# Performance work log

Hardware: AMD Instinct MI355X
Metric: run time of the kernel (lower is better)

The kernel has to match this reference:

```python
import jax, jax.numpy as jnp
import numpy as np

B, C, K, P = 32, 32, 3, 4
PSIZE = P * P
STRIDE = 2
EPS = 1e-8
BN_EPS = 1e-5


def _bn(x, scale, bias, mean, var):
    # eval-mode BatchNorm over channel-last axis
    return (x - mean) * (scale / jnp.sqrt(var + BN_EPS)) + bias


def setup_inputs() -> dict:
    key = jax.random.key(0)
    ks = jax.random.split(key, 13)
    b, h, w = 8, 64, 64
    c1_in, c1_out = C * K * K * 16, C * K * K      # 4608 -> 288
    c2_in, c2_out = C * K * K * 17, C * 17         # 4896 -> 544
    return {
        "x": jax.random.normal(ks[0], (b, B * (PSIZE + 1), h, w), jnp.float32),
        "weights": jax.random.normal(ks[1], (1, 1, C, B + 1), jnp.float32),
        "gamma": jax.random.normal(ks[2], (1, 1, 1, B, 1), jnp.float32),
        "conv1_w": jax.random.normal(ks[3], (c1_out, c1_in), jnp.float32) * 0.02,
        "bn1_scale": jax.random.uniform(ks[4], (c1_out,), jnp.float32) + 0.5,
        "bn1_bias": jax.random.normal(ks[5], (c1_out,), jnp.float32) * 0.1,
        "bn1_mean": jax.random.normal(ks[6], (c1_out,), jnp.float32) * 0.1,
        "bn1_var": jax.random.uniform(ks[7], (c1_out,), jnp.float32) + 0.5,
        "conv2_w": jax.random.normal(ks[8], (c2_out, c2_in), jnp.float32) * 0.02,
        "bn2_scale": jax.random.uniform(ks[9], (c2_out,), jnp.float32) + 0.5,
        "bn2_bias": jax.random.normal(ks[10], (c2_out,), jnp.float32) * 0.1,
        "bn2_mean": jax.random.normal(ks[11], (c2_out,), jnp.float32) * 0.1,
        "bn2_var": jax.random.uniform(ks[12], (c2_out,), jnp.float32) + 0.5,
    }


def reference(x, weights, gamma, conv1_w, bn1_scale, bn1_bias, bn1_mean, bn1_var,
              conv2_w, bn2_scale, bn2_bias, bn2_mean, bn2_var):
    b = x.shape[0]
    x = jnp.transpose(x, (0, 2, 3, 1))                       # (b,h,w,c)
    # add_pathes: zero-pad h,w by 1 then gather K*K overlapping patches
    x = jnp.pad(x, ((0, 0), (1, 1), (1, 1), (0, 0)))
    hp = x.shape[1]
    starts = np.arange(0, hp - K + 1, STRIDE)                # static
    idxs = starts[:, None] + np.arange(K)                    # (oh,K)
    oh = ow = int((hp - K) / STRIDE + 1)
    x = x[:, idxs]                                           # (b,oh,K,wp,c)
    x = x[:, :, :, idxs]                                     # (b,oh,K,ow,K,c)
    x = jnp.transpose(x, (0, 1, 3, 2, 4, 5))                 # (b,oh,ow,K,K,c)

    hw, kk = oh * ow, K * K
    p_in = x[..., :B * PSIZE].reshape(b, hw, kk, B, PSIZE)
    p_in = jnp.transpose(p_in, (0, 3, 1, 2, 4)).reshape(b, B, hw * kk * PSIZE)
    a_in = x[..., B * PSIZE:].reshape(b, hw, kk, B, 1)

    # transform_view: per-capsule-type normalization over all patches
    mu = p_in.mean(-1, keepdims=True)
    var = p_in.var(-1, ddof=1, keepdims=True)                # torch unbiased var
    p = (p_in - mu) / jnp.sqrt(var + EPS)                    # (b,B,N)
    p = jnp.transpose(p, (0, 2, 1)).reshape(b, hw, kk, B, PSIZE)
    p = a_in * p * gamma                                     # activation+gamma gating
    gsm = jax.nn.softmax(gamma, axis=3)                      # softmax over B
    psum = jnp.sum(p * gsm, axis=3, keepdims=True)           # (b,hw,kk,1,PSIZE)
    p = jnp.concatenate([p, psum], axis=3)                   # (b,hw,kk,B+1,PSIZE)
    w_sm = jax.nn.softmax(weights, axis=2)[0, 0]             # (C,B+1), softmax over C
    p_out = jnp.einsum('cd,bhkdp->bhkcp', w_sm, p)           # (b,hw,kk,C,PSIZE)
    p_out = p_out.reshape(b, oh, ow, kk * C * PSIZE)         # channels-last, 4608

    # conv1: 1x1 conv + BN + sigmoid
    a = jnp.einsum('bhwc,oc->bhwo', p_out, conv1_w)
    a = jax.nn.sigmoid(_bn(a, bn1_scale, bn1_bias, bn1_mean, bn1_var))
    out = jnp.concatenate([p_out, a], axis=3)                # 4896 channels
    # conv2: 1x1 conv + BN + relu
    y = jnp.einsum('bhwc,oc->bhwo', out, conv2_w)
    y = jax.nn.relu(_bn(y, bn2_scale, bn2_bias, bn2_mean, bn2_var))
    return jnp.transpose(y, (0, 3, 1, 2))                    # (b, C*17, oh, ow)
```

## Files before the change

### kernel.cpp

```cpp
#include <hip/hip_runtime.h>
#include <math.h>


typedef unsigned short u16;
typedef __attribute__((ext_vector_type(8))) short short8;
typedef __attribute__((ext_vector_type(4))) float f32x4;
typedef __attribute__((ext_vector_type(16))) float f32x16;

#define MFMA16(a, b, c) __builtin_amdgcn_mfma_f32_16x16x32_bf16(a, b, c, 0, 0, 0)
#define MFMA32(a, b, c) __builtin_amdgcn_mfma_f32_32x32x16_bf16(a, b, c, 0, 0, 0)
#define SB0() __builtin_amdgcn_sched_barrier(0)

#define LN_EPS 1e-8f

#define O_MU    0
#define O_RSTD  256
#define O_W2    512
#define O_BN1S  1536
#define O_BN1B  1824
#define O_BN2S  2112
#define O_BN2B  2656
#define O_ZB    3200

#define O_G_B     16384ull
#define O_AACT_B  (O_G_B + 33554432ull)
#define O_PART_B  (O_AACT_B + 5242880ull)
#define O_WF_B    (O_PART_B + 17825792ull)
#define O_WA_B    (O_WF_B + 9437184ull)

__device__ __forceinline__ u16 f2bf(float f) {
  union { float f; unsigned u; } v; v.f = f;
  unsigned r = (v.u + 0x7fffu + ((v.u >> 16) & 1u)) >> 16;
  return (u16)r;
}

__device__ __forceinline__ void gll16(const void* g, void* l) {
  __builtin_amdgcn_global_load_lds(
      (const __attribute__((address_space(1))) unsigned int*)g,
      (__attribute__((address_space(3))) unsigned int*)l, 16, 0, 0);
}

__device__ __forceinline__ int sfun(int r) { return (r >> 1) & 3; }

__global__ __launch_bounds__(256) void prep_kernel(
    const float* __restrict__ wts, const float* __restrict__ gamma,
    const float* __restrict__ bn1s, const float* __restrict__ bn1bi,
    const float* __restrict__ bn1m, const float* __restrict__ bn1v,
    const float* __restrict__ bn2s, const float* __restrict__ bn2bi,
    const float* __restrict__ bn2m, const float* __restrict__ bn2v,
    float* __restrict__ ws)
{
  __shared__ float wsm[32 * 33];
  __shared__ float gs[32];
  int t = threadIdx.x;
  if (t < 33) {
    float mx = -1e30f;
    for (int c = 0; c < 32; ++c) mx = fmaxf(mx, wts[c * 33 + t]);
    float sum = 0.f;
    for (int c = 0; c < 32; ++c) {
      float e = expf(wts[c * 33 + t] - mx);
      wsm[c * 33 + t] = e; sum += e;
    }
    float inv = 1.f / sum;
    for (int c = 0; c < 32; ++c) wsm[c * 33 + t] *= inv;
  }
  if (t == 64) {
    float mx = -1e30f;
    for (int d = 0; d < 32; ++d) mx = fmaxf(mx, gamma[d]);
    for (int d = 0; d < 32; ++d) { float e = expf(gamma[d] - mx); gs[d] = e; }
    float sum = 0.f;
    for (int d = 0; d < 32; ++d) sum += gs[d];
    float inv = 1.f / sum;
    for (int d = 0; d < 32; ++d) gs[d] *= inv;
  }
  __syncthreads();
  for (int i = t; i < 1024; i += 256) {
    int c = i >> 5, d = i & 31;
    ws[O_W2 + i] = (wsm[c * 33 + d] + wsm[c * 33 + 32] * gs[d]) * gamma[d];
  }
  for (int i = t; i < 288; i += 256) {
    float s = bn1s[i] / sqrtf(bn1v[i] + 1e-5f);
    ws[O_BN1S + i] = s;
    ws[O_BN1B + i] = bn1bi[i] - bn1m[i] * s;
  }
  for (int i = t; i < 544; i += 256) {
    float s = bn2s[i] / sqrtf(bn2v[i] + 1e-5f);
    ws[O_BN2S + i] = s;
    ws[O_BN2B + i] = bn2bi[i] - bn2m[i] * s;
  }
  if (t < 64) ws[O_ZB + t] = 0.f;
}

__global__ __launch_bounds__(1024) void stats_kernel(
    const float* __restrict__ x, float* __restrict__ ws, u16* __restrict__ Aact)
{
  int g = blockIdx.x;
  int b = g >> 5, cb = g & 31;
  const float* base = x + (((size_t)(b * 544 + cb * 16)) << 12);
  float s = 0.f, q = 0.f;
  for (int idx = threadIdx.x; idx < 65536; idx += 1024) {
    int p = idx & 4095;
    int hi = p >> 6, wi = p & 63;
    float wh = ((hi & 1) && hi != 63) ? 2.f : 1.f;
    float ww = ((wi & 1) && wi != 63) ? 2.f : 1.f;
    float v = base[idx];
    float wgt = wh * ww;
    s += wgt * v;
    q += wgt * v * v;
  }
  __shared__ float sb[1024], qb[1024];
  int t = threadIdx.x;
  sb[t] = s; qb[t] = q;
  __syncthreads();
  for (int off = 512; off > 0; off >>= 1) {
    if (t < off) { sb[t] += sb[t + off]; qb[t] += qb[t + off]; }
    __syncthreads();
  }
  if (t == 0) {
    const float N = 147456.f;
    float mean = sb[0] / N;
    float var = (qb[0] - sb[0] * sb[0] / N) / (N - 1.f);
    ws[O_MU + g] = mean;
    ws[O_RSTD + g] = 1.f / sqrtf(var + LN_EPS);
  }
  {
    int pos = (g << 5) + (t >> 5);
    Aact[(size_t)pos * 320 + 288 + (t & 31)] = 0;
  }
}

__global__ __launch_bounds__(256) void wcvt_kernel(
    const float* __restrict__ w1, const float* __restrict__ w2,
    const float* __restrict__ wsf, u16* __restrict__ Wf)
{
  __shared__ float rowl[512];
  __shared__ float w2l[1024];
  int bid = blockIdx.x;
  int o = bid / 9, tap = bid - (bid / 9) * 9;
  int t = threadIdx.x;
  int nt = o >> 7, cc = o & 127;
  if (o < 832) {
    const float* src = (o < 288)
        ? (w1 + (size_t)o * 4608 + tap * 512)
        : (w2 + (size_t)(o - 288) * 4896 + tap * 512);
    rowl[t] = src[t];
    rowl[t + 256] = src[t + 256];
    w2l[t] = wsf[O_W2 + t];
    w2l[t + 256] = wsf[O_W2 + t + 256];
    w2l[t + 512] = wsf[O_W2 + t + 512];
    w2l[t + 768] = wsf[O_W2 + t + 768];
    __syncthreads();
#pragma unroll
    for (int i = 0; i < 2; ++i) {
      int j = (t << 1) + i;
      int d = j >> 4, ps = j & 15;
      float s = 0.f;
#pragma unroll
      for (int c = 0; c < 32; ++c)
        s = fmaf(rowl[(c << 4) + ps], w2l[(c << 5) + d], s);
      int ch = (tap << 4) + (j >> 5);
      int kin = j & 31;
      int p = (kin >> 3) ^ ((cc >> 1) & 3);
      size_t idx = ((((size_t)(nt * 144 + ch)) * 128 + cc) * 4 + p) * 8 + (kin & 7);
      Wf[idx] = f2bf(s);
    }
  } else {
#pragma unroll
    for (int i = 0; i < 2; ++i) {
      int j = (t << 1) + i;
      int ch = (tap << 4) + (j >> 5);
      int kin = j & 31;
      int p = (kin >> 3) ^ ((cc >> 1) & 3);
      size_t idx = ((((size_t)(nt * 144 + ch)) * 128 + cc) * 4 + p) * 8 + (kin & 7);
      Wf[idx] = 0;
    }
  }
}

__global__ __launch_bounds__(256) void wa_cvt_kernel(
    const float* __restrict__ w2, u16* __restrict__ Wa)
{
  int s2 = blockIdx.x * 256 + threadIdx.x;
  int cb = s2 / 768, si = s2 - cb * 768;
  int ob = cb / 5, ch = cb - ob * 5;
  int nt = si >> 8, ks = (si >> 6) & 3, l2 = si & 63;
  int o = ob * 96 + (nt << 5) + (l2 & 31);
  int kf = (ch << 6) + (ks << 4) + ((l2 >> 5) << 3);
  u16* dst = Wa + (size_t)s2 * 8;
#pragma unroll
  for (int e = 0; e < 8; ++e) {
    int k = kf + e;
    float v = (o < 544 && k < 288) ? w2[(size_t)o * 4896 + 4608 + k] : 0.f;
    dst[e] = f2bf(v);
  }
}

__global__ __launch_bounds__(256) void g_kernel(
    const float* __restrict__ x, const float* __restrict__ ws,
    u16* __restrict__ Ub)
{
  __shared__ __align__(16) float raw[16][545];
  __shared__ __align__(16) float ut[16][576];
  __shared__ float mus[32], rss[32];
  int t = threadIdx.x;
  int pb = blockIdx.x;
  int b = pb >> 8, hi = (pb >> 2) & 63, wi0 = (pb & 3) << 4;

  {
    int ch4 = t >> 2, wl4 = (t & 3) << 2;
    size_t gbase = ((size_t)b * 544) << 12;
    size_t rowoff = ((size_t)hi << 6) + (size_t)(wi0 + wl4);
    for (int it = 0; it < 9; ++it) {
      int ch = it * 64 + ch4;
      if (ch < 544) {
        float4 v = *reinterpret_cast<const float4*>(
            &x[gbase + ((size_t)ch << 12) + rowoff]);
        raw[wl4 + 0][ch] = v.x;
        raw[wl4 + 1][ch] = v.y;
        raw[wl4 + 2][ch] = v.z;
        raw[wl4 + 3][ch] = v.w;
      }
    }
  }
  if (t < 32) { mus[t] = ws[O_MU + b * 32 + t]; rss[t] = ws[O_RSTD + b * 32 + t]; }
  __syncthreads();

  {
    int dl = t & 15, psp = t >> 4;
    for (int it = 0; it < 32; ++it) {
      int pix = it >> 1, half = it & 1;
      int dp = half * 16 + dl;
      int j = (dp << 4) + psp;
      int cbv = j & 31, psv = j >> 5;
      float val = (raw[pix][(cbv << 4) + psv] - mus[cbv]) * rss[cbv];
      ut[pix][psp * 36 + dp] = raw[pix][512 + dp] * val;
    }
  }
  __syncthreads();

  {
    u16* Up = Ub + ((size_t)((((b << 6) + hi) << 6) + wi0)) * 512;
    int j0 = t << 1;
    int a0 = (j0 & 15) * 36 + (j0 >> 4);
    int a1 = ((j0 + 1) & 15) * 36 + ((j0 + 1) >> 4);
    for (int pix = 0; pix < 16; ++pix) {
      float v0 = ut[pix][a0];
      float v1 = ut[pix][a1];
      unsigned pack = (unsigned)f2bf(v0) | ((unsigned)f2bf(v1) << 16);
      *reinterpret_cast<unsigned*>(Up + (size_t)pix * 512 + j0) = pack;
    }
  }
}

__global__ __launch_bounds__(256) void gemm_fused(
    const u16* __restrict__ Ubp, const u16* __restrict__ Wf,
    const float* __restrict__ wsf, u16* __restrict__ Aact,
    float* __restrict__ partC2)
{
  __shared__ __align__(16) u16 AlA[3][4096];
  __shared__ __align__(16) u16 AlB[3][4096];
  const int t = threadIdx.x;
  const int w = t >> 6, l = t & 63;
  const int wtm = w & 1, wtn = w >> 1;
  int bx = blockIdx.x;
  int xcd = bx & 7, idx = bx >> 3;
  int mloc = idx & 7, nt = idx >> 3;
  int mt = (xcd << 3) + mloc;
  int p0 = mt << 7;

  size_t pixb[2]; int hb[2], wb[2], qa[2], dof[2];
#pragma unroll
  for (int g = 0; g < 2; ++g) {
    int r = (w << 5) + (g << 4) + (l >> 2);
    int pos = p0 + r;
    int b_ = pos >> 10, h_ = (pos >> 5) & 31, w_ = pos & 31;
    pixb[g] = ((size_t)b_) << 12;
    hb[g] = 2 * h_ - 1;
    wb[g] = 2 * w_ - 1;
    qa[g] = (((l & 3) ^ sfun(r)) << 3);
    dof[g] = ((w << 5) + (g << 4)) * 32 + (l << 3);
  }
  const u16* zb = (const u16*)(wsf + O_ZB);
  const u16* wfslab = Wf + ((size_t)(nt * 144)) * 4096;

  int aoffs[4], boffs[4];
#pragma unroll
  for (int f = 0; f < 4; ++f) {
    int r = (wtm << 6) + (f << 4) + (l & 15);
    aoffs[f] = r * 32 + ((((l >> 4)) ^ sfun(r)) << 3);
    int c = (wtn << 6) + (f << 4) + (l & 15);
    boffs[f] = c * 32 + ((((l >> 4)) ^ sfun(c)) << 3);
  }

  f32x4 acc[4][4];
#pragma unroll
  for (int i = 0; i < 4; ++i)
#pragma unroll
    for (int j = 0; j < 4; ++j) acc[i][j] = (f32x4){0.f, 0.f, 0.f, 0.f};

  auto stage = [&](int ch, int buf) {
    int tap = ch >> 4;
    int kh = tap / 3, kw = tap - kh * 3;
    int cbase = (ch & 15) << 5;
#pragma unroll
    for (int g = 0; g < 2; ++g) {
      int hi = hb[g] + kh, wi = wb[g] + kw;
      bool ok = ((unsigned)hi < 64u) && ((unsigned)wi < 64u);
      const u16* src = ok
          ? (Ubp + ((pixb[g] + ((size_t)hi << 6) + (size_t)wi) << 9) + cbase + qa[g])
          : (zb + qa[g]);
      gll16(src, &AlA[buf][dof[g]]);
    }
    const u16* wsrc = wfslab + ((size_t)ch << 12);
#pragma unroll
    for (int g = 0; g < 2; ++g)
      gll16(wsrc + dof[g], &AlB[buf][dof[g]]);
  };

  stage(0, 0);
  stage(1, 1);

  int buf = 0;
  for (int n = 0; n < 144; ++n) {
    SB0();
    if (n < 143) asm volatile("s_waitcnt vmcnt(4)" ::: "memory");
    else         asm volatile("s_waitcnt vmcnt(0)" ::: "memory");
    SB0();
    __builtin_amdgcn_s_barrier();
    SB0();
    if (n + 2 < 144) {
      int nb = (buf >= 1) ? buf - 1 : 2;
      stage(n + 2, nb);
    }
    SB0();
    short8 aF[4], bF[4];
#pragma unroll
    for (int f = 0; f < 4; ++f) {
      aF[f] = *(const short8*)&AlA[buf][aoffs[f]];
      bF[f] = *(const short8*)&AlB[buf][boffs[f]];
    }
    __builtin_amdgcn_s_setprio(1);
#pragma unroll
    for (int fm = 0; fm < 4; ++fm)
#pragma unroll
      for (int fn = 0; fn < 4; ++fn)
        acc[fm][fn] = MFMA16(aF[fm], bF[fn], acc[fm][fn]);
    __builtin_amdgcn_s_setprio(0);
    buf = (buf == 2) ? 0 : buf + 1;
  }

  const float* s1 = wsf + O_BN1S;
  const float* b1 = wsf + O_BN1B;
#pragma unroll
  for (int fn = 0; fn < 4; ++fn) {
    int o = nt * 128 + (wtn << 6) + (fn << 4) + (l & 15);
    if (o < 288) {
      float sc = s1[o], bi = b1[o];
#pragma unroll
      for (int fm = 0; fm < 4; ++fm) {
        int posr = p0 + (wtm << 6) + (fm << 4) + ((l >> 4) << 2);
#pragma unroll
        for (int r = 0; r < 4; ++r) {
          float z = acc[fm][fn][r] * sc + bi;
          float sg = 1.f / (1.f + expf(-z));
          Aact[(size_t)(posr + r) * 320 + o] = f2bf(sg);
        }
      }
    } else if (o < 832) {
#pragma unroll
      for (int fm = 0; fm < 4; ++fm) {
        int posr = p0 + (wtm << 6) + (fm << 4) + ((l >> 4) << 2);
#pragma unroll
        for (int r = 0; r < 4; ++r)
          partC2[(size_t)(posr + r) * 544 + (o - 288)] = acc[fm][fn][r];
      }
    }
  }
}

__global__ __launch_bounds__(256, 2) void gemm_act(
    const u16* __restrict__ Aact, const u16* __restrict__ Wa,
    const float* __restrict__ partial, const float* __restrict__ wsf,
    float* __restrict__ outp)
{
  __shared__ __align__(16) char lraw[57344];
  u16 (*AlA)[128 * 64] = (u16 (*)[128 * 64])lraw;
  u16 (*AlB)[6144] = (u16 (*)[6144])(lraw + 32768);
  float* T = (float*)lraw;
  const int t = threadIdx.x;
  const int wid = t >> 6, l = t & 63;
  int bx = blockIdx.x;
  int xcd = bx & 7, idx = bx >> 3;
  int mt = xcd + ((idx & 7) << 3);
  int ob = idx >> 3;
  int p0 = mt << 7;

  const u16* abase[4];
  int srow[4];
#pragma unroll
  for (int s = 0; s < 4; ++s) {
    int r = (wid << 5) + (s << 3) + (l >> 3);
    int jsw = ((l & 7) ^ (r & 7)) << 3;
    srow[s] = (wid << 5) + (s << 3);
    abase[s] = Aact + (size_t)(p0 + r) * 320 + jsw;
  }
  const u16* wslice = Wa + (size_t)(ob * 5) * 6144;
  const int bsub = (wid << 9) + (l << 3);

  f32x16 acc0 = {}, acc1 = {}, acc2 = {};

  auto stageA = [&](int ch, u16* lbuf) {
#pragma unroll
    for (int s = 0; s < 4; ++s)
      gll16(abase[s] + (ch << 6), lbuf + (srow[s] << 6));
  };
  auto stageB = [&](int ch, u16* lbuf) {
    const u16* src = wslice + (size_t)ch * 6144 + bsub;
#pragma unroll
    for (int c = 0; c < 3; ++c)
      gll16(src + (c << 11), lbuf + (c << 11) + (wid << 9));
  };
  const int rr = (wid << 5) + (l & 31);
  auto ldsA = [&](const u16* lbuf, short8* av) {
#pragma unroll
    for (int ks = 0; ks < 4; ++ks) {
      int jl = (ks << 1) + (l >> 5);
      av[ks] = *(const short8*)(lbuf + (rr << 6) + ((jl ^ (rr & 7)) << 3));
    }
  };
  auto ldsB = [&](const u16* lbuf, short8* bf) {
#pragma unroll
    for (int k2 = 0; k2 < 12; ++k2)
      bf[k2] = *(const short8*)(lbuf + (k2 << 9) + (l << 3));
  };
  auto mfmaR = [&](const short8* av, const short8* bf) {
    __builtin_amdgcn_s_setprio(1);
#pragma unroll
    for (int ks = 0; ks < 4; ++ks) {
      acc0 = MFMA32(av[ks], bf[ks], acc0);
      acc1 = MFMA32(av[ks], bf[4 + ks], acc1);
      acc2 = MFMA32(av[ks], bf[8 + ks], acc2);
    }
    __builtin_amdgcn_s_setprio(0);
  };

  short8 av[4], bf[12];

  stageA(0, AlA[0]);
  stageB(0, AlB[0]);
  asm volatile("s_waitcnt vmcnt(0)" ::: "memory");
  __builtin_amdgcn_s_barrier();

#define APHASE(K, CUR, NXT)                                                   \
  SB0();                                                                      \
  if ((K) + 1 < 5) { stageA((K) + 1, AlA[NXT]); stageB((K) + 1, AlB[NXT]); }  \
  SB0();                                                                      \
  ldsA(AlA[CUR], av);                                                         \
  ldsB(AlB[CUR], bf);                                                         \
  SB0();                                                                      \
  mfmaR(av, bf);                                                              \
  SB0();                                                                      \
  asm volatile("s_waitcnt vmcnt(0)" ::: "memory");                            \
  __builtin_amdgcn_s_barrier();

  APHASE(0, 0, 1);
  APHASE(1, 1, 0);
  APHASE(2, 0, 1);
  APHASE(3, 1, 0);
  APHASE(4, 0, 1);
#undef APHASE

  __syncthreads();

  const float* s2p = wsf + O_BN2S;
  const float* b2p = wsf + O_BN2B;
#pragma unroll
  for (int nt = 0; nt < 3; ++nt) {
    int ol = (nt << 5) + (l & 31);
    int o = ob * 96 + ol;
    float sc = 0.f, bi = 0.f;
    if (o < 544) { sc = s2p[o]; bi = b2p[o]; }
    f32x16 a = (nt == 0) ? acc0 : ((nt == 1) ? acc1 : acc2);
#pragma unroll
    for (int reg = 0; reg < 16; ++reg) {
      int rowD = (reg & 3) + ((reg >> 2) << 3) + ((l >> 5) << 2);
      int pos = p0 + (wid << 5) + rowD;
      float pz = 0.f;
      if (o < 544) pz = partial[(size_t)pos * 544 + o];
      float z = (a[reg] + pz) * sc + bi;
      T[ol * 129 + (wid << 5) + rowD] = fmaxf(z, 0.f);
    }
  }
  __syncthreads();
  for (int s2 = t; s2 < 3072; s2 += 256) {
    int ol = s2 >> 5, c4 = s2 & 31;
    int o = ob * 96 + ol;
    if (o < 544) {
      int pos0 = p0 + (c4 << 2);
      int bb = pos0 >> 10, hw0 = pos0 & 1023;
      int base = ol * 129 + (c4 << 2);
      float4 v;
      v.x = T[base]; v.y = T[base + 1]; v.z = T[base + 2]; v.w = T[base + 3];
      *(float4*)&outp[(((size_t)(bb * 544 + o)) << 10) + hw0] = v;
    }
  }
}

extern "C" void kernel_launch(void* const* d_in, const int* in_sizes, int n_in,
                              void* d_out, int out_size, void* d_ws,
                              size_t ws_size, hipStream_t stream)
{
  const float* x       = (const float*)d_in[0];
  const float* wts     = (const float*)d_in[1];
  const float* gamma   = (const float*)d_in[2];
  const float* conv1_w = (const float*)d_in[3];
  const float* bn1s    = (const float*)d_in[4];
  const float* bn1b    = (const float*)d_in[5];
  const float* bn1m    = (const float*)d_in[6];
  const float* bn1v    = (const float*)d_in[7];
  const float* conv2_w = (const float*)d_in[8];
  const float* bn2s    = (const float*)d_in[9];
  const float* bn2b    = (const float*)d_in[10];
  const float* bn2m    = (const float*)d_in[11];
  const float* bn2v    = (const float*)d_in[12];

  char* wsb = (char*)d_ws;
  float* wsf = (float*)d_ws;
  u16* Ub    = (u16*)(wsb + O_G_B);
  u16* Aact  = (u16*)(wsb + O_AACT_B);
  float* prt = (float*)(wsb + O_PART_B);
  u16* Wf    = (u16*)(wsb + O_WF_B);
  u16* Wa    = (u16*)(wsb + O_WA_B);
  float* out = (float*)d_out;

  prep_kernel<<<1, 256, 0, stream>>>(wts, gamma, bn1s, bn1b, bn1m, bn1v,
                                     bn2s, bn2b, bn2m, bn2v, wsf);
  stats_kernel<<<256, 1024, 0, stream>>>(x, wsf, Aact);
  wcvt_kernel<<<9216, 256, 0, stream>>>(conv1_w, conv2_w, wsf, Wf);
  wa_cvt_kernel<<<90, 256, 0, stream>>>(conv2_w, Wa);
  g_kernel<<<2048, 256, 0, stream>>>(x, wsf, Ub);
  gemm_fused<<<512, 256, 0, stream>>>(Ub, Wf, wsf, Aact, prt);
  gemm_act<<<384, 256, 0, stream>>>(Aact, Wa, prt, wsf, out);
}
```

Measured before the change: 205.5 us.

## Merge preprocessing kernels into one launch and halve gemm_act tile height

Result: slower. 214.5 us (+4.4%).

```diff
diff --git a/kernel.cpp b/kernel.cpp
--- a/kernel.cpp
+++ b/kernel.cpp
@@ -42,156 +42,168 @@
 
 __device__ __forceinline__ int sfun(int r) { return (r >> 1) & 3; }
 
-__global__ __launch_bounds__(256) void prep_kernel(
+__global__ __launch_bounds__(1024) void aux_kernel(
+    const float* __restrict__ x,
     const float* __restrict__ wts, const float* __restrict__ gamma,
+    const float* __restrict__ w1, const float* __restrict__ w2,
     const float* __restrict__ bn1s, const float* __restrict__ bn1bi,
     const float* __restrict__ bn1m, const float* __restrict__ bn1v,
     const float* __restrict__ bn2s, const float* __restrict__ bn2bi,
     const float* __restrict__ bn2m, const float* __restrict__ bn2v,
-    float* __restrict__ ws)
+    float* __restrict__ ws, u16* __restrict__ Aact,
+    u16* __restrict__ Wf, u16* __restrict__ Wa)
 {
-  __shared__ float wsm[32 * 33];
-  __shared__ float gs[32];
+  __shared__ __align__(16) char shm[12800];
+  int bid = blockIdx.x;
   int t = threadIdx.x;
-  if (t < 33) {
-    float mx = -1e30f;
-    for (int c = 0; c < 32; ++c) mx = fmaxf(mx, wts[c * 33 + t]);
-    float sum = 0.f;
-    for (int c = 0; c < 32; ++c) {
-      float e = expf(wts[c * 33 + t] - mx);
-      wsm[c * 33 + t] = e; sum += e;
-    }
-    float inv = 1.f / sum;
-    for (int c = 0; c < 32; ++c) wsm[c * 33 + t] *= inv;
-  }
-  if (t == 64) {
-    float mx = -1e30f;
-    for (int d = 0; d < 32; ++d) mx = fmaxf(mx, gamma[d]);
-    for (int d = 0; d < 32; ++d) { float e = expf(gamma[d] - mx); gs[d] = e; }
-    float sum = 0.f;
-    for (int d = 0; d < 32; ++d) sum += gs[d];
-    float inv = 1.f / sum;
-    for (int d = 0; d < 32; ++d) gs[d] *= inv;
-  }
-  __syncthreads();
-  for (int i = t; i < 1024; i += 256) {
-    int c = i >> 5, d = i & 31;
-    ws[O_W2 + i] = (wsm[c * 33 + d] + wsm[c * 33 + 32] * gs[d]) * gamma[d];
-  }
-  for (int i = t; i < 288; i += 256) {
-    float s = bn1s[i] / sqrtf(bn1v[i] + 1e-5f);
-    ws[O_BN1S + i] = s;
-    ws[O_BN1B + i] = bn1bi[i] - bn1m[i] * s;
-  }
-  for (int i = t; i < 544; i += 256) {
-    float s = bn2s[i] / sqrtf(bn2v[i] + 1e-5f);
-    ws[O_BN2S + i] = s;
-    ws[O_BN2B + i] = bn2bi[i] - bn2m[i] * s;
-  }
-  if (t < 64) ws[O_ZB + t] = 0.f;
-}
-
-__global__ __launch_bounds__(1024) void stats_kernel(
-    const float* __restrict__ x, float* __restrict__ ws, u16* __restrict__ Aact)
-{
-  int g = blockIdx.x;
-  int b = g >> 5, cb = g & 31;
-  const float* base = x + (((size_t)(b * 544 + cb * 16)) << 12);
-  float s = 0.f, q = 0.f;
-  for (int idx = threadIdx.x; idx < 65536; idx += 1024) {
-    int p = idx & 4095;
-    int hi = p >> 6, wi = p & 63;
-    float wh = ((hi & 1) && hi != 63) ? 2.f : 1.f;
-    float ww = ((wi & 1) && wi != 63) ? 2.f : 1.f;
-    float v = base[idx];
-    float wgt = wh * ww;
-    s += wgt * v;
-    q += wgt * v * v;
-  }
-  __shared__ float sb[1024], qb[1024];
-  int t = threadIdx.x;
-  sb[t] = s; qb[t] = q;
-  __syncthreads();
-  for (int off = 512; off > 0; off >>= 1) {
-    if (t < off) { sb[t] += sb[t + off]; qb[t] += qb[t + off]; }
+
+  if (bid == 0) {
+    float* wsm = (float*)shm;
+    float* gs = wsm + 1056;
+    if (t < 33) {
+      float mx = -1e30f;
+      for (int c = 0; c < 32; ++c) mx = fmaxf(mx, wts[c * 33 + t]);
+      float sum = 0.f;
+      for (int c = 0; c < 32; ++c) {
+        float e = expf(wts[c * 33 + t] - mx);
+        wsm[c * 33 + t] = e; sum += e;
+      }
+      float inv = 1.f / sum;
+      for (int c = 0; c < 32; ++c) wsm[c * 33 + t] *= inv;
+    }
+    if (t == 64) {
+      float mx = -1e30f;
+      for (int d = 0; d < 32; ++d) mx = fmaxf(mx, gamma[d]);
+      for (int d = 0; d < 32; ++d) gs[d] = expf(gamma[d] - mx);
+      float sum = 0.f;
+      for (int d = 0; d < 32; ++d) sum += gs[d];
+      float inv = 1.f / sum;
+      for (int d = 0; d < 32; ++d) gs[d] *= inv;
+    }
     __syncthreads();
-  }
-  if (t == 0) {
-    const float N = 147456.f;
-    float mean = sb[0] / N;
-    float var = (qb[0] - sb[0] * sb[0] / N) / (N - 1.f);
-    ws[O_MU + g] = mean;
-    ws[O_RSTD + g] = 1.f / sqrtf(var + LN_EPS);
-  }
-  {
-    int pos = (g << 5) + (t >> 5);
-    Aact[(size_t)pos * 320 + 288 + (t & 31)] = 0;
-  }
-}
-
-__global__ __launch_bounds__(256) void wcvt_kernel(
-    const float* __restrict__ w1, const float* __restrict__ w2,
-    const float* __restrict__ wsf, u16* __restrict__ Wf)
-{
-  __shared__ float rowl[512];
-  __shared__ float w2l[1024];
-  int bid = blockIdx.x;
-  int o = bid / 9, tap = bid - (bid / 9) * 9;
-  int t = threadIdx.x;
-  int nt = o >> 7, cc = o & 127;
-  if (o < 832) {
-    const float* src = (o < 288)
-        ? (w1 + (size_t)o * 4608 + tap * 512)
-        : (w2 + (size_t)(o - 288) * 4896 + tap * 512);
-    rowl[t] = src[t];
-    rowl[t + 256] = src[t + 256];
-    w2l[t] = wsf[O_W2 + t];
-    w2l[t + 256] = wsf[O_W2 + t + 256];
-    w2l[t + 512] = wsf[O_W2 + t + 512];
-    w2l[t + 768] = wsf[O_W2 + t + 768];
+    {
+      int c = t >> 5, d = t & 31;
+      ws[O_W2 + t] = (wsm[c * 33 + d] + wsm[c * 33 + 32] * gs[d]) * gamma[d];
+    }
+    if (t < 288) {
+      float s = bn1s[t] / sqrtf(bn1v[t] + 1e-5f);
+      ws[O_BN1S + t] = s;
+      ws[O_BN1B + t] = bn1bi[t] - bn1m[t] * s;
+    }
+    if (t < 544) {
+      float s = bn2s[t] / sqrtf(bn2v[t] + 1e-5f);
+      ws[O_BN2S + t] = s;
+      ws[O_BN2B + t] = bn2bi[t] - bn2m[t] * s;
+    }
+    if (t < 64) ws[O_ZB + t] = 0.f;
+  } else if (bid <= 256) {
+    int g = bid - 1;
+    int b = g >> 5, cb = g & 31;
+    const float* base = x + (((size_t)(b * 544 + cb * 16)) << 12);
+    float s = 0.f, q = 0.f;
+    for (int idx = t; idx < 65536; idx += 1024) {
+      int p = idx & 4095;
+      int hi = p >> 6, wi = p & 63;
+      float wh = ((hi & 1) && hi != 63) ? 2.f : 1.f;
+      float ww = ((wi & 1) && wi != 63) ? 2.f : 1.f;
+      float v = base[idx];
+      float wgt = wh * ww;
+      s += wgt * v;
+      q += wgt * v * v;
+    }
+    float* sb = (float*)shm;
+    float* qb = sb + 1024;
+    sb[t] = s; qb[t] = q;
     __syncthreads();
-#pragma unroll
-    for (int i = 0; i < 2; ++i) {
-      int j = (t << 1) + i;
+    for (int off = 512; off > 0; off >>= 1) {
+      if (t < off) { sb[t] += sb[t + off]; qb[t] += qb[t + off]; }
+      __syncthreads();
+    }
+    if (t == 0) {
+      const float N = 147456.f;
+      float mean = sb[0] / N;
+      float var = (qb[0] - sb[0] * sb[0] / N) / (N - 1.f);
+      ws[O_MU + g] = mean;
+      ws[O_RSTD + g] = 1.f / sqrtf(var + LN_EPS);
+    }
+    {
+      int pos = (g << 5) + (t >> 5);
+      Aact[(size_t)pos * 320 + 288 + (t & 31)] = 0;
+    }
+  } else if (bid < 4865) {
+    float* rowl = (float*)shm;
+    float* wsm = rowl + 1024;
+    float* gs = wsm + 1056;
+    float* w2l = gs + 32;
+    int pid = bid - 257;
+    int half = t >> 9, tl = t & 511;
+    int slot = (pid << 1) + half;
+    int o = slot / 9, tap = slot - 9 * o;
+    int nt = o >> 7, cc = o & 127;
+    if (t < 33) {
+      float mx = -1e30f;
+      for (int c = 0; c < 32; ++c) mx = fmaxf(mx, wts[c * 33 + t]);
+      float sum = 0.f;
+      for (int c = 0; c < 32; ++c) {
+        float e = expf(wts[c * 33 + t] - mx);
+        wsm[c * 33 + t] = e; sum += e;
+      }
+      float inv = 1.f / sum;
+      for (int c = 0; c < 32; ++c) wsm[c * 33 + t] *= inv;
+    }
+    if (t == 64) {
+      float mx = -1e30f;
+      for (int d = 0; d < 32; ++d) mx = fmaxf(mx, gamma[d]);
+      for (int d = 0; d < 32; ++d) gs[d] = expf(gamma[d] - mx);
+      float sum = 0.f;
+      for (int d = 0; d < 32; ++d) sum += gs[d];
+      float inv = 1.f / sum;
+      for (int d = 0; d < 32; ++d) gs[d] *= inv;
+    }
+    if (o < 832) {
+      const float* src = (o < 288)
+          ? (w1 + (size_t)o * 4608 + tap * 512)
+          : (w2 + (size_t)(o - 288) * 4896 + tap * 512);
+      rowl[(half << 9) + tl] = src[tl];
+    }
+    __syncthreads();
+    {
+      int c = t >> 5, d = t & 31;
+      w2l[t] = (wsm[c * 33 + d] + wsm[c * 33 + 32] * gs[d]) * gamma[d];
+    }
+    __syncthreads();
+    {
+      int j = tl;
       int d = j >> 4, ps = j & 15;
       float s = 0.f;
-#pragma unroll
-      for (int c = 0; c < 32; ++c)
-        s = fmaf(rowl[(c << 4) + ps], w2l[(c << 5) + d], s);
+      if (o < 832) {
+        const float* rl = rowl + (half << 9);
+#pragma unroll
+        for (int c = 0; c < 32; ++c)
+          s = fmaf(rl[(c << 4) + ps], w2l[(c << 5) + d], s);
+      }
       int ch = (tap << 4) + (j >> 5);
       int kin = j & 31;
       int p = (kin >> 3) ^ ((cc >> 1) & 3);
       size_t idx = ((((size_t)(nt * 144 + ch)) * 128 + cc) * 4 + p) * 8 + (kin & 7);
-      Wf[idx] = f2bf(s);
+      Wf[idx] = (o < 832) ? f2bf(s) : (u16)0;
     }
   } else {
-#pragma unroll
-    for (int i = 0; i < 2; ++i) {
-      int j = (t << 1) + i;
-      int ch = (tap << 4) + (j >> 5);
-      int kin = j & 31;
-      int p = (kin >> 3) ^ ((cc >> 1) & 3);
-      size_t idx = ((((size_t)(nt * 144 + ch)) * 128 + cc) * 4 + p) * 8 + (kin & 7);
-      Wf[idx] = 0;
-    }
-  }
-}
-
-__global__ __launch_bounds__(256) void wa_cvt_kernel(
-    const float* __restrict__ w2, u16* __restrict__ Wa)
-{
-  int s2 = blockIdx.x * 256 + threadIdx.x;
-  int cb = s2 / 768, si = s2 - cb * 768;
-  int ob = cb / 5, ch = cb - ob * 5;
-  int nt = si >> 8, ks = (si >> 6) & 3, l2 = si & 63;
-  int o = ob * 96 + (nt << 5) + (l2 & 31);
-  int kf = (ch << 6) + (ks << 4) + ((l2 >> 5) << 3);
-  u16* dst = Wa + (size_t)s2 * 8;
-#pragma unroll
-  for (int e = 0; e < 8; ++e) {
-    int k = kf + e;
-    float v = (o < 544 && k < 288) ? w2[(size_t)o * 4896 + 4608 + k] : 0.f;
-    dst[e] = f2bf(v);
+    int s2 = (bid - 4865) * 1024 + t;
+    if (s2 < 23040) {
+      int cb = s2 / 768, si = s2 - cb * 768;
+      int ob = cb / 5, ch = cb - ob * 5;
+      int nt = si >> 8, ks = (si >> 6) & 3, l2 = si & 63;
+      int o = ob * 96 + (nt << 5) + (l2 & 31);
+      int kf = (ch << 6) + (ks << 4) + ((l2 >> 5) << 3);
+      u16* dst = Wa + (size_t)s2 * 8;
+#pragma unroll
+      for (int e = 0; e < 8; ++e) {
+        int k = kf + e;
+        float v = (o < 544 && k < 288) ? w2[(size_t)o * 4896 + 4608 + k] : 0.f;
+        dst[e] = f2bf(v);
+      }
+    }
   }
 }
 
@@ -378,22 +390,22 @@
   }
 }
 
-__global__ __launch_bounds__(256, 2) void gemm_act(
+__global__ __launch_bounds__(128) void gemm_act(
     const u16* __restrict__ Aact, const u16* __restrict__ Wa,
     const float* __restrict__ partial, const float* __restrict__ wsf,
     float* __restrict__ outp)
 {
-  __shared__ __align__(16) char lraw[57344];
-  u16 (*AlA)[128 * 64] = (u16 (*)[128 * 64])lraw;
-  u16 (*AlB)[6144] = (u16 (*)[6144])(lraw + 32768);
+  __shared__ __align__(16) char lraw[40960];
+  u16 (*AlA)[4096] = (u16 (*)[4096])lraw;
+  u16 (*AlB)[6144] = (u16 (*)[6144])(lraw + 16384);
   float* T = (float*)lraw;
   const int t = threadIdx.x;
   const int wid = t >> 6, l = t & 63;
   int bx = blockIdx.x;
   int xcd = bx & 7, idx = bx >> 3;
-  int mt = xcd + ((idx & 7) << 3);
-  int ob = idx >> 3;
-  int p0 = mt << 7;
+  int mloc = idx & 15, ob = idx >> 4;
+  int mt = (xcd << 4) + mloc;
+  int p0 = mt << 6;
 
   const u16* abase[4];
   int srow[4];
@@ -415,10 +427,10 @@
       gll16(abase[s] + (ch << 6), lbuf + (srow[s] << 6));
   };
   auto stageB = [&](int ch, u16* lbuf) {
-    const u16* src = wslice + (size_t)ch * 6144 + bsub;
-#pragma unroll
-    for (int c = 0; c < 3; ++c)
-      gll16(src + (c << 11), lbuf + (c << 11) + (wid << 9));
+    const u16* src = wslice + (size_t)ch * 6144;
+#pragma unroll
+    for (int c = 0; c < 6; ++c)
+      gll16(src + (c << 10) + bsub, lbuf + (c << 10) + bsub);
   };
   const int rr = (wid << 5) + (l & 31);
   auto ldsA = [&](const u16* lbuf, short8* av) {
@@ -488,17 +500,17 @@
       float pz = 0.f;
       if (o < 544) pz = partial[(size_t)pos * 544 + o];
       float z = (a[reg] + pz) * sc + bi;
-      T[ol * 129 + (wid << 5) + rowD] = fmaxf(z, 0.f);
+      T[ol * 65 + (wid << 5) + rowD] = fmaxf(z, 0.f);
     }
   }
   __syncthreads();
-  for (int s2 = t; s2 < 3072; s2 += 256) {
-    int ol = s2 >> 5, c4 = s2 & 31;
+  for (int s2 = t; s2 < 1536; s2 += 128) {
+    int ol = s2 >> 4, c4 = s2 & 15;
     int o = ob * 96 + ol;
     if (o < 544) {
       int pos0 = p0 + (c4 << 2);
       int bb = pos0 >> 10, hw0 = pos0 & 1023;
-      int base = ol * 129 + (c4 << 2);
+      int base = ol * 65 + (c4 << 2);
       float4 v;
       v.x = T[base]; v.y = T[base + 1]; v.z = T[base + 2]; v.w = T[base + 3];
       *(float4*)&outp[(((size_t)(bb * 544 + o)) << 10) + hw0] = v;
@@ -533,12 +545,11 @@
   u16* Wa    = (u16*)(wsb + O_WA_B);
   float* out = (float*)d_out;
 
-  prep_kernel<<<1, 256, 0, stream>>>(wts, gamma, bn1s, bn1b, bn1m, bn1v,
-                                     bn2s, bn2b, bn2m, bn2v, wsf);
-  stats_kernel<<<256, 1024, 0, stream>>>(x, wsf, Aact);
-  wcvt_kernel<<<9216, 256, 0, stream>>>(conv1_w, conv2_w, wsf, Wf);
-  wa_cvt_kernel<<<90, 256, 0, stream>>>(conv2_w, Wa);
+  aux_kernel<<<4888, 1024, 0, stream>>>(x, wts, gamma, conv1_w, conv2_w,
+                                        bn1s, bn1b, bn1m, bn1v,
+                                        bn2s, bn2b, bn2m, bn2v,
+                                        wsf, Aact, Wf, Wa);
   g_kernel<<<2048, 256, 0, stream>>>(x, wsf, Ub);
   gemm_fused<<<512, 256, 0, stream>>>(Ub, Wf, wsf, Aact, prt);
-  gemm_act<<<384, 256, 0, stream>>>(Aact, Wa, prt, wsf, out);
-}
+  gemm_act<<<768, 128, 0, stream>>>(Aact, Wa, prt, wsf, out);
+}
```
